# Performance work log

Hardware: AMD Instinct MI355X
Metric: run time of the kernel (lower is better)

Reference implementation:

```python
import jax, jax.numpy as jnp
import numpy as np

# Matches the torch constant: 1/sqrt(2*3.14159) (NOT math.pi)
INV_SQRT_2PI = 1.0 / np.sqrt(np.float32(2.0 * 3.14159))


def density_ir_normal(x):
    return INV_SQRT_2PI * jnp.exp(-0.5 * x * x)


def setup_inputs() -> dict:
    key = jax.random.key(0)
    k1, k2, k3 = jax.random.split(key, 3)
    batch = 8388608           # 2**23 output slots
    n_events = 16777216       # 2**24 scattered events (avg 2 per slot)
    idx = jax.random.randint(k1, (n_events,), 0, batch)
    vals = jax.random.normal(k2, (n_events,), dtype=jnp.float32)
    # theta0 in (0,1) (branch prob), theta1 > 0 (scale), theta2 (loc)
    thetas = jnp.array([0.7, 1.3, 0.2], dtype=jnp.float32)
    return {"batch": batch, "idx": idx, "vals": vals, "thetas": thetas}


def reference(batch, idx, vals, thetas):
    # l_4_high = min(thetas[0], 1); l_5 = max(l_4_high, 0) -> clip(theta0, 0, 1)
    l_5_lhs_integral = jnp.clip(thetas[0], 0.0, 1.0)
    l_1_cond = 1.0 - l_5_lhs_integral
    # per-event multiplicative factor (vectorized density evaluation)
    z = (vals - thetas[2]) / thetas[1]
    factors = (1.0 - l_1_cond) * density_ir_normal(z) / thetas[1]
    # multiplicative scatter; duplicate indices multiply in (matches the
    # sequential result[idx[i]] *= factor loop, product is order-invariant)
    result = jnp.ones(batch, dtype=vals.dtype).at[idx].multiply(factors)
    return result * l_1_cond
```

## Files before the change

kernel.cpp:

```cpp
#include <hip/hip_runtime.h>
#include <climits>


#define INV_SQRT_2PI 0.39894246f
#define SLOT_BITS 14
#define SLOTS (1 << SLOT_BITS)
#define NB_MAX 512
#define NBLK 512
#define BTHREADS 512
#define TILE 2048
#define STAGE_S 28
#define QSCALE 8192.0f
#define QMASK 0x3FFFFu

#define LDS_BAR() do {                                        \
    asm volatile("s_waitcnt lgkmcnt(0)" ::: "memory");        \
    __builtin_amdgcn_s_barrier();                             \
} while (0)

__device__ __forceinline__ long long region_idx(int blk, int b, int nbuckets,
                                                int swzmask) {
    int bb = swzmask ? ((b + blk) & swzmask) : b;
    return (long long)blk * nbuckets + bb;
}

__device__ __forceinline__ void ovf_push(uint2* ovf, int* ovf_cnt, int ovcap,
                                         unsigned gslot, unsigned q) {
    int op = atomicAdd(ovf_cnt, 1);
    if (op < ovcap) ovf[op] = make_uint2(gslot, q);
}

struct Ev4 { int4 k; float4 v; int cnt; };

__device__ __forceinline__ Ev4 load4(const int* __restrict__ idx,
                                     const float* __restrict__ vals,
                                     long long base, long long te) {
    Ev4 r; r.cnt = 0;
    r.k = make_int4(0,0,0,0); r.v = make_float4(0,0,0,0);
    if (base + 4 <= te) {
        r.k = *(const int4*)(idx + base);
        r.v = *(const float4*)(vals + base);
        r.cnt = 4;
    } else if (base < te) {
        int c = (int)(te - base);
        int kk[4] = {0,0,0,0}; float vv[4] = {0,0,0,0};
        for (int i = 0; i < c; ++i) { kk[i] = idx[base+i]; vv[i] = vals[base+i]; }
        r.k = make_int4(kk[0],kk[1],kk[2],kk[3]);
        r.v = make_float4(vv[0],vv[1],vv[2],vv[3]);
        r.cnt = c;
    }
    return r;
}

__global__ __launch_bounds__(BTHREADS) void bin_kernel(
        const int* __restrict__ idx, const float* __restrict__ vals,
        const float* __restrict__ thetas,
        unsigned* __restrict__ pairs,
        int* __restrict__ fill,
        uint2* __restrict__ ovf, int* __restrict__ ovf_cnt, int ovcap,
        int n, int nbuckets, int cap_shift, int swzmask, int epb) {
    __shared__ unsigned stage[NB_MAX * STAGE_S];
    __shared__ int scnt[NB_MAX];
    __shared__ int cnum[NB_MAX];

    const int tid = threadIdx.x;
    const int blk = blockIdx.x;
    const int cappb = 1 << cap_shift;
    long long start = (long long)blk * epb;
    long long end = start + epb;
    if (end > n) end = n;

    for (int b = tid; b < nbuckets; b += BTHREADS) { scnt[b] = 0; cnum[b] = 0; }
    __syncthreads();

    const float t1 = thetas[1], t2 = thetas[2];
    const float t0c = fminf(fmaxf(thetas[0], 0.0f), 1.0f);
    const float inv_t1 = 1.0f / t1;

    Ev4 cur; cur.cnt = 0;
    if (start < end) {
        long long te0 = start + TILE; if (te0 > end) te0 = end;
        cur = load4(idx, vals, start + (long long)tid * 4, te0);
    }

    for (long long ts = start; ts < end; ts += TILE) {
        Ev4 nxt; nxt.cnt = 0;
        long long tsn = ts + TILE;
        if (tsn < end) {
            long long ten = tsn + TILE; if (ten > end) ten = end;
            nxt = load4(idx, vals, tsn + (long long)tid * 4, ten);
        }

        int   kk[4] = {cur.k.x, cur.k.y, cur.k.z, cur.k.w};
        float vv[4] = {cur.v.x, cur.v.y, cur.v.z, cur.v.w};
        int bs[4]; unsigned recs[4]; int pos[4];
        #pragma unroll
        for (int j = 0; j < 4; ++j) {
            unsigned uk = (unsigned)kk[j];
            bs[j] = (int)(uk >> SLOT_BITS);
            float z = (vv[j] - t2) * inv_t1;
            float u = 0.5f * z * z;
            unsigned q = __float2uint_rn(fminf(u * QSCALE, (float)QMASK));
            recs[j] = ((uk & (SLOTS - 1)) << 18) | q;
        }
        #pragma unroll
        for (int j = 0; j < 4; ++j) {
            pos[j] = (j < cur.cnt && bs[j] < nbuckets)
                     ? atomicAdd(&scnt[bs[j]], 1) : INT_MAX;
        }
        #pragma unroll
        for (int j = 0; j < 4; ++j) {
            if (pos[j] == INT_MAX) continue;
            if (pos[j] < STAGE_S) stage[bs[j] * STAGE_S + pos[j]] = recs[j];
            else ovf_push(ovf, ovf_cnt, ovcap, (unsigned)kk[j], recs[j] & QMASK);
        }
        LDS_BAR();

        for (int b = tid; b < nbuckets; b += BTHREADS) {
            int c = scnt[b]; if (c > STAGE_S) c = STAGE_S;
            if (c >= 16) {
                int have = cnum[b];
                if (have < (cappb >> 4)) {
                    unsigned* dst = pairs +
                        (region_idx(blk, b, nbuckets, swzmask) << cap_shift) + (have << 4);
                    const uint4* s4 = (const uint4*)&stage[b * STAGE_S];
                    uint4* d4 = (uint4*)dst;
                    d4[0]=s4[0]; d4[1]=s4[1]; d4[2]=s4[2]; d4[3]=s4[3];
                    cnum[b] = have + 1;
                    int rem = c - 16;
                    for (int i = 0; i < rem; ++i)
                        stage[b*STAGE_S + i] = stage[b*STAGE_S + 16 + i];
                    scnt[b] = rem;
                } else {
                    for (int i = 0; i < c; ++i) {
                        unsigned r = stage[b*STAGE_S + i];
                        ovf_push(ovf, ovf_cnt, ovcap,
                                 ((unsigned)b << SLOT_BITS) | (r >> 18), r & QMASK);
                    }
                    scnt[b] = 0;
                }
            } else scnt[b] = c;
        }
        LDS_BAR();
        cur = nxt;
    }

    for (int b = tid; b < nbuckets; b += BTHREADS) {
        int c = scnt[b]; if (c > STAGE_S) c = STAGE_S;
        int have = cnum[b];
        int valid = have << 4;
        int nfull = (c + 15) >> 4;
        int fit = (cappb >> 4) - have;
        int nw = nfull < fit ? nfull : fit;
        if (nw > 0) {
            unsigned* dst = pairs +
                (region_idx(blk, b, nbuckets, swzmask) << cap_shift) + (have << 4);
            const uint4* s4 = (const uint4*)&stage[b * STAGE_S];
            uint4* d4 = (uint4*)dst;
            for (int ch = 0; ch < nw; ++ch) {
                d4[ch*4+0]=s4[ch*4+0]; d4[ch*4+1]=s4[ch*4+1];
                d4[ch*4+2]=s4[ch*4+2]; d4[ch*4+3]=s4[ch*4+3];
            }
            int v2 = nw << 4; if (v2 > c) v2 = c;
            valid += v2;
        }
        for (int i = (nw << 4); i < c; ++i) {
            unsigned r = stage[b*STAGE_S + i];
            ovf_push(ovf, ovf_cnt, ovcap,
                     ((unsigned)b << SLOT_BITS) | (r >> 18), r & QMASK);
        }
        fill[region_idx(blk, b, nbuckets, swzmask)] = valid;
    }
}

__global__ __launch_bounds__(1024) void reduce_kernel(
        const unsigned* __restrict__ pairs, const int* __restrict__ fill,
        const uint2* __restrict__ ovf, const int* __restrict__ ovf_cnt, int ovcap,
        const float* __restrict__ thetas, float* __restrict__ out,
        long long n_out, int nbuckets, int cap_shift, int swzmask) {
    __shared__ unsigned accu[SLOTS];
    const int tid = threadIdx.x;
    const int b = blockIdx.x;

    for (int s = tid; s < SLOTS; s += 1024) accu[s] = 0u;
    __syncthreads();

    const int wave = tid >> 6, lane = tid & 63;
    const int SEGS = NBLK / 16;

    int sl = wave + (lane & 31) * 16;
    int cntv = fill[region_idx(sl, b, nbuckets, swzmask)];

    const unsigned* pc = pairs +
        (region_idx(wave, b, nbuckets, swzmask) << cap_shift);
    unsigned a0 = pc[lane];
    unsigned a1 = pc[64 + lane];

    for (int i = 0; i < SEGS; ++i) {
        const unsigned* pn = pc; unsigned n0 = 0, n1 = 0;
        if (i < SEGS - 1) {
            int sn = wave + (i + 1) * 16;
            pn = pairs + (region_idx(sn, b, nbuckets, swzmask) << cap_shift);
            n0 = pn[lane];
            n1 = pn[64 + lane];
        }
        int ca = __builtin_amdgcn_readlane(cntv, i);
        if (lane < ca)      atomicAdd(&accu[a0 >> 18], (1u << 25) + (a0 & QMASK));
        if (64 + lane < ca) atomicAdd(&accu[a1 >> 18], (1u << 25) + (a1 & QMASK));
        for (int r = 128 + lane; r < ca; r += 64) {
            unsigned rec = pc[r];
            atomicAdd(&accu[rec >> 18], (1u << 25) + (rec & QMASK));
        }
        pc = pn; a0 = n0; a1 = n1;
    }
    __syncthreads();

    int no = *ovf_cnt; if (no > ovcap) no = ovcap;
    for (int i = tid; i < no; i += 1024) {
        uint2 e = ovf[i];
        if ((int)(e.x >> SLOT_BITS) == b)
            atomicAdd(&accu[e.x & (SLOTS - 1)], (1u << 25) + e.y);
    }
    __syncthreads();

    const float t1 = thetas[1];
    const float t0c = fminf(fmaxf(thetas[0], 0.0f), 1.0f);
    const float logC = logf(t0c * INV_SQRT_2PI / t1);
    const float cond = 1.0f - t0c;
    long long obase = (long long)b << SLOT_BITS;
    for (int ss = tid; ss < SLOTS; ss += 1024) {
        long long o = obase + ss;
        if (o < n_out) {
            unsigned av = accu[ss];
            float v = (float)(av >> 25) * logC
                    - (float)(av & 0x1FFFFFFu) * (1.0f / QSCALE);
            out[o] = cond * expf(v);
        }
    }
}

__global__ void init_zero_kernel(float* __restrict__ out, int n) {
    int i = blockIdx.x * blockDim.x + threadIdx.x;
    int stride = gridDim.x * blockDim.x;
    for (; i < n; i += stride) out[i] = 0.0f;
}
__global__ void scatter_log_kernel(const int* __restrict__ idx,
                                   const float* __restrict__ vals,
                                   const float* __restrict__ thetas,
                                   float* __restrict__ acc, int n) {
    float t1 = thetas[1], t2 = thetas[2];
    float t0c = fminf(fmaxf(thetas[0], 0.0f), 1.0f);
    float logC = logf(t0c * INV_SQRT_2PI / t1);
    float inv_t1 = 1.0f / t1;
    int i = blockIdx.x * blockDim.x + threadIdx.x;
    int stride = gridDim.x * blockDim.x;
    for (; i < n; i += stride) {
        float z = (vals[i] - t2) * inv_t1;
        atomicAdd(&acc[idx[i]], fmaf(-0.5f * z, z, logC));
    }
}
__global__ void finalize_kernel(float* __restrict__ out,
                                const float* __restrict__ thetas, int n) {
    float t0c = fminf(fmaxf(thetas[0], 0.0f), 1.0f);
    float cond = 1.0f - t0c;
    int i = blockIdx.x * blockDim.x + threadIdx.x;
    int stride = gridDim.x * blockDim.x;
    for (; i < n; i += stride) out[i] = cond * expf(out[i]);
}

extern "C" void kernel_launch(void* const* d_in, const int* in_sizes, int n_in,
                              void* d_out, int out_size, void* d_ws, size_t ws_size,
                              hipStream_t stream) {
    const int*   idx    = (const int*)d_in[1];
    const float* vals   = (const float*)d_in[2];
    const float* thetas = (const float*)d_in[3];
    float*       out    = (float*)d_out;

    int n_events = in_sizes[1];
    long long n_out = out_size;
    int nbuckets = (int)((n_out + SLOTS - 1) >> SLOT_BITS);

    long long tiles_total = ((long long)n_events + TILE - 1) / TILE;
    long long tpb = (tiles_total + NBLK - 1) / NBLK;
    int epb = (int)(tpb * TILE);
    long long avg = nbuckets > 0 ? (epb + nbuckets - 1) / nbuckets : 1;
    long long want = avg + avg / 2 + 32;
    int cap_shift = 6;
    while ((1LL << cap_shift) < want && cap_shift < 20) ++cap_shift;
    long long cappb = 1LL << cap_shift;
    int swzmask = (nbuckets > 0 && (nbuckets & (nbuckets - 1)) == 0)
                  ? nbuckets - 1 : 0;

    size_t pairs_b = (size_t)NBLK * nbuckets * cappb * 4;
    size_t fill_b  = (size_t)NBLK * nbuckets * 4;
    size_t head    = pairs_b + fill_b + 64;
    bool fast = (nbuckets > 0) && (nbuckets <= NB_MAX) && (n_events > 0) &&
                (ws_size >= head + 64 * 1024);

    if (fast) {
        unsigned* pairs = (unsigned*)d_ws;
        int* fill = (int*)((char*)d_ws + pairs_b);
        int* ovf_cnt = (int*)((char*)d_ws + pairs_b + fill_b);
        uint2* ovf = (uint2*)((char*)d_ws + head);
        long long ovcap_ll = (long long)((ws_size - head) / 8);
        int ovcap = (int)(ovcap_ll > 4194304 ? 4194304 : ovcap_ll);

        hipMemsetAsync(ovf_cnt, 0, sizeof(int), stream);
        bin_kernel<<<NBLK, BTHREADS, 0, stream>>>(idx, vals, thetas, pairs, fill,
                                                  ovf, ovf_cnt, ovcap,
                                                  n_events, nbuckets, cap_shift,
                                                  swzmask, epb);
        reduce_kernel<<<nbuckets, 1024, 0, stream>>>(pairs, fill, ovf, ovf_cnt,
                                                     ovcap, thetas, out,
                                                     n_out, nbuckets, cap_shift,
                                                     swzmask);
    } else {
        const int BLOCK = 256;
        int grid_out = min((int)((n_out + BLOCK - 1) / BLOCK), 2048);
        int grid_ev  = min((n_events + BLOCK - 1) / BLOCK, 2048);
        init_zero_kernel<<<grid_out, BLOCK, 0, stream>>>(out, (int)n_out);
        scatter_log_kernel<<<grid_ev, BLOCK, 0, stream>>>(idx, vals, thetas, out, n_events);
        finalize_kernel<<<grid_out, BLOCK, 0, stream>>>(out, thetas, (int)n_out);
    }
}
```

Baseline: 100.3 us.

## Replace linear LDS staging with swizzled ring buffers and double the tile size

The per-bucket LDS staging array, which shifted leftover records down after each 16-record flush, becomes a 32-entry ring buffer per bucket. Flushes now copy a half-ring without compacting, and the slot index is XOR-swizzled to spread LDS bank accesses. Each thread now loads 8 events per tile instead of 4, giving tiles of 4096 events and half as many barrier rounds. The cost is more registers for the double-buffered 8-event prefetch, plus new ring-window bookkeeping that overflows records once a ring is full.

```diff
diff --git a/kernel.cpp b/kernel.cpp
--- a/kernel.cpp
+++ b/kernel.cpp
@@ -8,8 +8,8 @@
 #define NB_MAX 512
 #define NBLK 512
 #define BTHREADS 512
-#define TILE 2048
-#define STAGE_S 28
+#define TILE 4096
+#define RING 32
 #define QSCALE 8192.0f
 #define QMASK 0x3FFFFu
 
@@ -24,32 +24,14 @@
     return (long long)blk * nbuckets + bb;
 }
 
+__device__ __forceinline__ int ring_slot(int b, int pos) {
+    return b * RING + ((pos & (RING - 1)) ^ ((b & 7) << 2));
+}
+
 __device__ __forceinline__ void ovf_push(uint2* ovf, int* ovf_cnt, int ovcap,
                                          unsigned gslot, unsigned q) {
     int op = atomicAdd(ovf_cnt, 1);
     if (op < ovcap) ovf[op] = make_uint2(gslot, q);
-}
-
-struct Ev4 { int4 k; float4 v; int cnt; };
-
-__device__ __forceinline__ Ev4 load4(const int* __restrict__ idx,
-                                     const float* __restrict__ vals,
-                                     long long base, long long te) {
-    Ev4 r; r.cnt = 0;
-    r.k = make_int4(0,0,0,0); r.v = make_float4(0,0,0,0);
-    if (base + 4 <= te) {
-        r.k = *(const int4*)(idx + base);
-        r.v = *(const float4*)(vals + base);
-        r.cnt = 4;
-    } else if (base < te) {
-        int c = (int)(te - base);
-        int kk[4] = {0,0,0,0}; float vv[4] = {0,0,0,0};
-        for (int i = 0; i < c; ++i) { kk[i] = idx[base+i]; vv[i] = vals[base+i]; }
-        r.k = make_int4(kk[0],kk[1],kk[2],kk[3]);
-        r.v = make_float4(vv[0],vv[1],vv[2],vv[3]);
-        r.cnt = c;
-    }
-    return r;
 }
 
 __global__ __launch_bounds__(BTHREADS) void bin_kernel(
@@ -59,7 +41,7 @@
         int* __restrict__ fill,
         uint2* __restrict__ ovf, int* __restrict__ ovf_cnt, int ovcap,
         int n, int nbuckets, int cap_shift, int swzmask, int epb) {
-    __shared__ unsigned stage[NB_MAX * STAGE_S];
+    __shared__ unsigned ring[NB_MAX * RING];
     __shared__ int scnt[NB_MAX];
     __shared__ int cnum[NB_MAX];
 
@@ -77,25 +59,56 @@
     const float t0c = fminf(fmaxf(thetas[0], 0.0f), 1.0f);
     const float inv_t1 = 1.0f / t1;
 
-    Ev4 cur; cur.cnt = 0;
-    if (start < end) {
+    int   kk[8]; float vv[8]; int cnt_ev = 0;
+    int   nk[8]; float nv[8];
+    {
         long long te0 = start + TILE; if (te0 > end) te0 = end;
-        cur = load4(idx, vals, start + (long long)tid * 4, te0);
+        long long base = start + (long long)tid * 8;
+        if (base + 8 <= te0) {
+            int4 k0 = *(const int4*)(idx + base);
+            int4 k1 = *(const int4*)(idx + base + 4);
+            float4 v0 = *(const float4*)(vals + base);
+            float4 v1 = *(const float4*)(vals + base + 4);
+            kk[0]=k0.x;kk[1]=k0.y;kk[2]=k0.z;kk[3]=k0.w;
+            kk[4]=k1.x;kk[5]=k1.y;kk[6]=k1.z;kk[7]=k1.w;
+            vv[0]=v0.x;vv[1]=v0.y;vv[2]=v0.z;vv[3]=v0.w;
+            vv[4]=v1.x;vv[5]=v1.y;vv[6]=v1.z;vv[7]=v1.w;
+            cnt_ev = 8;
+        } else if (base < te0) {
+            cnt_ev = (int)(te0 - base);
+            #pragma unroll
+            for (int i = 0; i < 8; ++i) { kk[i] = 0; vv[i] = 0.0f; }
+            for (int i = 0; i < cnt_ev; ++i) { kk[i] = idx[base+i]; vv[i] = vals[base+i]; }
+        }
     }
 
     for (long long ts = start; ts < end; ts += TILE) {
-        Ev4 nxt; nxt.cnt = 0;
+        int nxt_cnt = 0;
         long long tsn = ts + TILE;
         if (tsn < end) {
             long long ten = tsn + TILE; if (ten > end) ten = end;
-            nxt = load4(idx, vals, tsn + (long long)tid * 4, ten);
-        }
-
-        int   kk[4] = {cur.k.x, cur.k.y, cur.k.z, cur.k.w};
-        float vv[4] = {cur.v.x, cur.v.y, cur.v.z, cur.v.w};
-        int bs[4]; unsigned recs[4]; int pos[4];
+            long long base = tsn + (long long)tid * 8;
+            if (base + 8 <= ten) {
+                int4 k0 = *(const int4*)(idx + base);
+                int4 k1 = *(const int4*)(idx + base + 4);
+                float4 v0 = *(const float4*)(vals + base);
+                float4 v1 = *(const float4*)(vals + base + 4);
+                nk[0]=k0.x;nk[1]=k0.y;nk[2]=k0.z;nk[3]=k0.w;
+                nk[4]=k1.x;nk[5]=k1.y;nk[6]=k1.z;nk[7]=k1.w;
+                nv[0]=v0.x;nv[1]=v0.y;nv[2]=v0.z;nv[3]=v0.w;
+                nv[4]=v1.x;nv[5]=v1.y;nv[6]=v1.z;nv[7]=v1.w;
+                nxt_cnt = 8;
+            } else if (base < ten) {
+                nxt_cnt = (int)(ten - base);
+                #pragma unroll
+                for (int i = 0; i < 8; ++i) { nk[i] = 0; nv[i] = 0.0f; }
+                for (int i = 0; i < nxt_cnt; ++i) { nk[i] = idx[base+i]; nv[i] = vals[base+i]; }
+            }
+        }
+
+        int bs[8]; unsigned recs[8]; int pos[8]; int win[8];
         #pragma unroll
-        for (int j = 0; j < 4; ++j) {
+        for (int j = 0; j < 8; ++j) {
             unsigned uk = (unsigned)kk[j];
             bs[j] = (int)(uk >> SLOT_BITS);
             float z = (vv[j] - t2) * inv_t1;
@@ -104,70 +117,77 @@
             recs[j] = ((uk & (SLOTS - 1)) << 18) | q;
         }
         #pragma unroll
-        for (int j = 0; j < 4; ++j) {
-            pos[j] = (j < cur.cnt && bs[j] < nbuckets)
-                     ? atomicAdd(&scnt[bs[j]], 1) : INT_MAX;
+        for (int j = 0; j < 8; ++j) {
+            bool ok = (j < cnt_ev) && (bs[j] < nbuckets);
+            win[j] = ok ? (cnum[bs[j]] << 4) : 0;
+            pos[j] = ok ? atomicAdd(&scnt[bs[j]], 1) : INT_MAX;
         }
         #pragma unroll
-        for (int j = 0; j < 4; ++j) {
+        for (int j = 0; j < 8; ++j) {
             if (pos[j] == INT_MAX) continue;
-            if (pos[j] < STAGE_S) stage[bs[j] * STAGE_S + pos[j]] = recs[j];
-            else ovf_push(ovf, ovf_cnt, ovcap, (unsigned)kk[j], recs[j] & QMASK);
+            if (pos[j] - win[j] < RING)
+                ring[ring_slot(bs[j], pos[j])] = recs[j];
+            else
+                ovf_push(ovf, ovf_cnt, ovcap, (unsigned)kk[j], recs[j] & QMASK);
         }
         LDS_BAR();
 
         for (int b = tid; b < nbuckets; b += BTHREADS) {
-            int c = scnt[b]; if (c > STAGE_S) c = STAGE_S;
-            if (c >= 16) {
-                int have = cnum[b];
-                if (have < (cappb >> 4)) {
-                    unsigned* dst = pairs +
-                        (region_idx(blk, b, nbuckets, swzmask) << cap_shift) + (have << 4);
-                    const uint4* s4 = (const uint4*)&stage[b * STAGE_S];
-                    uint4* d4 = (uint4*)dst;
+            int c = scnt[b];
+            int J = cnum[b];
+            int flushed = J << 4;
+            int stored_end = c < flushed + RING ? c : flushed + RING;
+            int navail = stored_end - flushed;
+            while (navail >= 16) {
+                int H = (J & 1) ^ ((b >> 2) & 1);
+                const uint4* s4 = (const uint4*)&ring[b * RING + (H << 4)];
+                if (J < (cappb >> 4)) {
+                    uint4* d4 = (uint4*)(pairs +
+                        (region_idx(blk, b, nbuckets, swzmask) << cap_shift) + (J << 4));
                     d4[0]=s4[0]; d4[1]=s4[1]; d4[2]=s4[2]; d4[3]=s4[3];
-                    cnum[b] = have + 1;
-                    int rem = c - 16;
-                    for (int i = 0; i < rem; ++i)
-                        stage[b*STAGE_S + i] = stage[b*STAGE_S + 16 + i];
-                    scnt[b] = rem;
                 } else {
-                    for (int i = 0; i < c; ++i) {
-                        unsigned r = stage[b*STAGE_S + i];
+                    for (int i = 0; i < 16; ++i) {
+                        unsigned r = ring[b * RING + (H << 4) + i];
                         ovf_push(ovf, ovf_cnt, ovcap,
                                  ((unsigned)b << SLOT_BITS) | (r >> 18), r & QMASK);
                     }
-                    scnt[b] = 0;
                 }
-            } else scnt[b] = c;
+                ++J; flushed += 16; navail -= 16;
+            }
+            cnum[b] = J;
+            if (c != stored_end) scnt[b] = stored_end;
         }
         LDS_BAR();
-        cur = nxt;
+
+        cnt_ev = nxt_cnt;
+        #pragma unroll
+        for (int j = 0; j < 8; ++j) { kk[j] = nk[j]; vv[j] = nv[j]; }
     }
 
     for (int b = tid; b < nbuckets; b += BTHREADS) {
-        int c = scnt[b]; if (c > STAGE_S) c = STAGE_S;
-        int have = cnum[b];
-        int valid = have << 4;
-        int nfull = (c + 15) >> 4;
-        int fit = (cappb >> 4) - have;
-        int nw = nfull < fit ? nfull : fit;
-        if (nw > 0) {
-            unsigned* dst = pairs +
-                (region_idx(blk, b, nbuckets, swzmask) << cap_shift) + (have << 4);
-            const uint4* s4 = (const uint4*)&stage[b * STAGE_S];
-            uint4* d4 = (uint4*)dst;
-            for (int ch = 0; ch < nw; ++ch) {
-                d4[ch*4+0]=s4[ch*4+0]; d4[ch*4+1]=s4[ch*4+1];
-                d4[ch*4+2]=s4[ch*4+2]; d4[ch*4+3]=s4[ch*4+3];
+        int c = scnt[b];
+        int J = cnum[b];
+        int flushed = J << 4;
+        int r = c - flushed;
+        int valid = flushed;
+        if (r > 0 && J < (cappb >> 4)) {
+            unsigned tmp[16];
+            int lbase = (J & 1) << 4;
+            #pragma unroll
+            for (int i = 0; i < 16; ++i)
+                tmp[i] = ring[b * RING + ((lbase + i) ^ ((b & 7) << 2))];
+            uint4* d4 = (uint4*)(pairs +
+                (region_idx(blk, b, nbuckets, swzmask) << cap_shift) + (J << 4));
+            const uint4* t4 = (const uint4*)tmp;
+            d4[0]=t4[0]; d4[1]=t4[1]; d4[2]=t4[2]; d4[3]=t4[3];
+            valid = flushed + r;
+        } else if (r > 0) {
+            int lbase = (J & 1) << 4;
+            for (int i = 0; i < r; ++i) {
+                unsigned rr = ring[b * RING + ((lbase + i) ^ ((b & 7) << 2))];
+                ovf_push(ovf, ovf_cnt, ovcap,
+                         ((unsigned)b << SLOT_BITS) | (rr >> 18), rr & QMASK);
             }
-            int v2 = nw << 4; if (v2 > c) v2 = c;
-            valid += v2;
-        }
-        for (int i = (nw << 4); i < c; ++i) {
-            unsigned r = stage[b*STAGE_S + i];
-            ovf_push(ovf, ovf_cnt, ovcap,
-                     ((unsigned)b << SLOT_BITS) | (r >> 18), r & QMASK);
         }
         fill[region_idx(blk, b, nbuckets, swzmask)] = valid;
     }
```

Measured after the change: 98.48 us. Within noise of the previous version (-1.9%).
